# Performance work log

Hardware: AMD Instinct MI355X
Metric: run time of the kernel (lower is better)

Reference implementation:

```python
import jax, jax.numpy as jnp
import numpy as np

B, A = 8192, 16
HID, NK, NQ, NV = 256, 32, 32, 128
IN_DIM, CUR_HID, CUR_OUT, N_ACT = 512, 512, 128, 64
EXT_LAMBD, INT_LAMBD = 1.0, 0.5


def setup_inputs() -> dict:
    key = jax.random.key(0)
    ks = jax.random.split(key, 16)
    def w(k, i, o):
        return jax.random.normal(k, (i, o), jnp.float32) / np.sqrt(i)
    return {
        'x': jax.random.normal(ks[0], (B * A, IN_DIM), jnp.float32),
        'hidden': jax.random.normal(ks[1], (B, A, HID), jnp.float32),
        'Wk': w(ks[2], HID, NK), 'bk': jnp.zeros((NK,), jnp.float32),
        'Wv': w(ks[3], HID, NV), 'bv': jnp.zeros((NV,), jnp.float32),
        'Wq': w(ks[4], HID, NQ), 'bq': jnp.zeros((NQ,), jnp.float32),
        'Wa': w(ks[5], NQ + NK * A, A), 'ba': jnp.zeros((A,), jnp.float32),
        'Wt1': w(ks[6], IN_DIM, CUR_HID), 'bt1': jnp.zeros((CUR_HID,), jnp.float32),
        'Wt2': w(ks[7], CUR_HID, CUR_OUT), 'bt2': jnp.zeros((CUR_OUT,), jnp.float32),
        'Wp1': w(ks[8], IN_DIM, CUR_HID), 'bp1': jnp.zeros((CUR_HID,), jnp.float32),
        'Wp2': w(ks[9], CUR_HID, CUR_HID), 'bp2': jnp.zeros((CUR_HID,), jnp.float32),
        'Wp3': w(ks[10], CUR_HID, CUR_OUT), 'bp3': jnp.zeros((CUR_OUT,), jnp.float32),
        'Wc': w(ks[11], NV + HID, HID), 'bc': jnp.zeros((HID,), jnp.float32),
        'W2': w(ks[12], HID, N_ACT), 'b2': jnp.zeros((N_ACT,), jnp.float32),
    }


def _aggregate(x, hidden, Wk, bk, Wv, bv, Wq, bq, Wa, ba, Wt1, bt1, Wt2, bt2,
               Wp1, bp1, Wp2, bp2, Wp3, bp3, Wc, bc, W2, b2):
    # communicate(): per-agent key / value / query projections
    key_ = hidden @ Wk + bk          # [B, A, NK]
    value = hidden @ Wv + bv         # [B, A, NV]
    query = hidden @ Wq + bq         # [B, A, NQ]
    # torch.cat([key[:, i, :] for i in range(A)], -1) == reshape; repeat == broadcast
    flat_key = key_.reshape(B, A * NK)
    qk = jnp.concatenate(
        [query, jnp.broadcast_to(flat_key[:, None, :], (B, A, A * NK))], axis=-1)
    attn_weights = jax.nn.softmax(qk @ Wa + ba, axis=-1)   # [B, A, A]
    # intrinsic-motivation predictors (dropout p=0.5 in eval mode -> identity)
    tar = jax.nn.relu(x @ Wt1 + bt1) @ Wt2 + bt2           # [B*A, CUR_OUT]
    pred = jax.nn.relu(x @ Wp1 + bp1)
    pred = jax.nn.relu(pred @ Wp2 + bp2)
    pred = pred @ Wp3 + bp3
    int_imp = jnp.mean((tar - pred) ** 2, axis=-1).reshape(B, A)
    int_imp = jax.nn.softmax(int_imp, axis=-1)             # [B, A]
    # view(B,A,1).repeat(1,1,A).permute(0,2,1): out[b,i,j] = int_imp[b,j]
    int_mat = jnp.broadcast_to(int_imp[:, None, :], (B, A, A))
    attn = EXT_LAMBD * attn_weights + INT_LAMBD * jax.lax.stop_gradient(int_mat)
    applied = jnp.einsum('bij,bjv->biv', attn, value)      # [B, A, NV]
    comb = jax.nn.relu(jnp.concatenate([applied, hidden], axis=-1) @ Wc + bc)
    return comb @ W2 + b2                                  # [B, A, N_ACT]


def reference(x, hidden, Wk, bk, Wv, bv, Wq, bq, Wa, ba, Wt1, bt1, Wt2, bt2,
              Wp1, bp1, Wp2, bp2, Wp3, bp3, Wc, bc, W2, b2):
    return _aggregate(x, hidden, Wk, bk, Wv, bv, Wq, bq, Wa, ba, Wt1, bt1,
                      Wt2, bt2, Wp1, bp1, Wp2, bp2, Wp3, bp3, Wc, bc, W2, b2)
```

## Files before the change

### kernel.cpp

```cpp
#include <hip/hip_runtime.h>
#include <cstddef>
#include <cstdint>

typedef unsigned short ushort_t;
typedef __attribute__((ext_vector_type(4))) float f32x4;
typedef __attribute__((ext_vector_type(8))) short bf16x8;

#define BB   8192
#define AA   16
#define BA   131072
#define HID  256
#define NV   128

__device__ __forceinline__ float bf2f(ushort_t u) {
    union { float f; uint32_t i; } v; v.i = ((uint32_t)u) << 16; return v.f;
}
__device__ __forceinline__ ushort_t f2bf(float f) {
    union { float f; uint32_t i; } v; v.f = f;
    uint32_t r = v.i + 0x7fffu + ((v.i >> 16) & 1u);
    return (ushort_t)(r >> 16);
}
__device__ __forceinline__ void gload_lds16(const void* g, void* l) {
    __builtin_amdgcn_global_load_lds(
        (const __attribute__((address_space(1))) uint32_t*)g,
        (__attribute__((address_space(3))) uint32_t*)l, 16, 0, 0);
}

__global__ __launch_bounds__(512)
void gemm256(const ushort_t* __restrict__ A, int lda,
             const ushort_t* __restrict__ A2, int lda2, int ksplit,
             const ushort_t* __restrict__ Bt,
             const float* __restrict__ bias,
             ushort_t* __restrict__ C, int ldc, int K, int lgx, int rpx)
{
    __shared__ ushort_t lds[65536];

    const int tid  = threadIdx.x;
    const int w    = tid >> 6;
    const int lane = tid & 63;
    const int wm   = w >> 2;
    const int wn   = w & 3;
    const int fr   = lane & 15;
    const int fq   = lane >> 4;

    const int bid  = blockIdx.x;
    const int xcd  = bid & 7;
    const int slot = bid >> 3;
    const int x    = slot & ((1 << lgx) - 1);
    const int y    = xcd * rpx + (slot >> lgx);
    const size_t brow = (size_t)y * 256;
    const int    bcol = x * 256;

    const int NT = K >> 5;

    f32x4 acc[8][4];
#pragma unroll
    for (int m = 0; m < 8; ++m)
#pragma unroll
        for (int n = 0; n < 4; ++n) acc[m][n] = (f32x4){0.f, 0.f, 0.f, 0.f};

    auto stage = [&](int buf, int k0) {
        const int base = buf << 14;
#pragma unroll
        for (int r = 0; r < 4; ++r) {
            const int gamma = r * 512 + tid;
            const int gi    = gamma & 1023;
            const int row   = gi >> 2;
            const int g     = gi & 3;
            const int s     = (row ^ (row >> 2)) & 3;
            const int col   = ((g ^ s) << 3);
            const ushort_t* src;
            if (gamma >= 1024) {
                src = Bt + (size_t)(bcol + row) * K + k0 + col;
            } else if (k0 >= ksplit) {
                src = A2 + (brow + row) * (size_t)lda2 + (k0 - ksplit) + col;
            } else {
                src = A  + (brow + row) * (size_t)lda  + k0 + col;
            }
            gload_lds16(src, &lds[base + gamma * 8]);
        }
    };

    stage(0, 0);
    if (NT > 1) stage(1, 32);
    if (NT > 2) stage(2, 64);

    const int sa = (fr ^ (fr >> 2)) & 3;
    const int pc = ((fq ^ sa) & 3) << 3;

    for (int t = 0; t < NT; ++t) {
        if (t + 3 <= NT)      asm volatile("s_waitcnt vmcnt(8)" ::: "memory");
        else if (t + 2 == NT) asm volatile("s_waitcnt vmcnt(4)" ::: "memory");
        else                  asm volatile("s_waitcnt vmcnt(0)" ::: "memory");
        __builtin_amdgcn_s_barrier();
        if (t + 3 < NT) stage((t + 3) & 3, (t + 3) << 5);

        const int base = (t & 3) << 14;
        bf16x8 a[8], b[4];
#pragma unroll
        for (int m = 0; m < 8; ++m)
            a[m] = *(const bf16x8*)&lds[base + (wm * 128 + m * 16 + fr) * 32 + pc];
#pragma unroll
        for (int n = 0; n < 4; ++n)
            b[n] = *(const bf16x8*)&lds[base + 8192 + (wn * 64 + n * 16 + fr) * 32 + pc];

        __builtin_amdgcn_s_setprio(1);
#pragma unroll
        for (int m = 0; m < 8; ++m)
#pragma unroll
            for (int n = 0; n < 4; ++n)
                acc[m][n] = __builtin_amdgcn_mfma_f32_16x16x32_bf16(
                    a[m], b[n], acc[m][n], 0, 0, 0);
        __builtin_amdgcn_s_setprio(0);
    }

#pragma unroll
    for (int m = 0; m < 8; ++m) {
        const size_t rowb = brow + wm * 128 + m * 16 + fq * 4;
#pragma unroll
        for (int n = 0; n < 4; ++n) {
            const int col = bcol + wn * 64 + n * 16 + fr;
            const float bv = bias[col];
#pragma unroll
            for (int r = 0; r < 4; ++r) {
                float v = fmaxf(acc[m][n][r] + bv, 0.f);
                C[(rowb + r) * (size_t)ldc + col] = f2bf(v);
            }
        }
    }
}

template<bool OBF16, bool RELU>
__global__ __launch_bounds__(256)
void gemm_mfma(const ushort_t* __restrict__ A, int lda,
               const ushort_t* __restrict__ A2, int lda2, int ksplit,
               const ushort_t* __restrict__ Bt,
               const float* __restrict__ bias,
               void* __restrict__ C, int ldc, int N, int K, int lgx)
{
    __shared__ ushort_t As[2][128 * 64];
    __shared__ ushort_t Bs[2][128 * 64];

    const int tid  = threadIdx.x;
    const int w    = tid >> 6;
    const int lane = tid & 63;
    const int wm   = w >> 1;
    const int wn   = w & 1;

    const int bid  = blockIdx.x;
    const int xcd  = bid & 7;
    const int slot = bid >> 3;
    const int x    = slot & ((1 << lgx) - 1);
    const int y    = xcd * 128 + (slot >> lgx);
    const size_t brow = (size_t)y * 128;
    const int    bcol = x * 128;

    const int fr   = lane & 15;
    const int fq   = lane >> 4;
    const int srow = lane >> 3;
    const int scol = (lane & 7) << 3;

    f32x4 acc[4][4];
#pragma unroll
    for (int i = 0; i < 4; ++i)
#pragma unroll
        for (int j = 0; j < 4; ++j) acc[i][j] = (f32x4){0.f, 0.f, 0.f, 0.f};

    const int NT = K >> 6;

    auto stage = [&](int buf, int k0) {
#pragma unroll
        for (int i = 0; i < 4; ++i) {
            const int c = (w << 2) + i;
            const int r = (c << 3) + srow;
            const ushort_t* asrc;
            if (k0 >= ksplit)
                asrc = A2 + (brow + r) * (size_t)lda2 + (k0 - ksplit) + scol;
            else
                asrc = A  + (brow + r) * (size_t)lda  + k0 + scol;
            gload_lds16(asrc, &As[buf][(c << 9) + lane * 8]);
            gload_lds16(Bt + (size_t)(bcol + r) * K + k0 + scol,
                        &Bs[buf][(c << 9) + lane * 8]);
        }
    };

    stage(0, 0);
    __syncthreads();

    for (int t = 0; t < NT; ++t) {
        const int cur = t & 1;
        if (t + 1 < NT) stage(cur ^ 1, (t + 1) << 6);
#pragma unroll
        for (int kk = 0; kk < 2; ++kk) {
            bf16x8 a[4], b[4];
#pragma unroll
            for (int f = 0; f < 4; ++f) {
                a[f] = *(const bf16x8*)&As[cur][(wm * 64 + f * 16 + fr) * 64 + kk * 32 + fq * 8];
                b[f] = *(const bf16x8*)&Bs[cur][(wn * 64 + f * 16 + fr) * 64 + kk * 32 + fq * 8];
            }
#pragma unroll
            for (int fm = 0; fm < 4; ++fm)
#pragma unroll
                for (int fn = 0; fn < 4; ++fn)
                    acc[fm][fn] = __builtin_amdgcn_mfma_f32_16x16x32_bf16(
                        a[fm], b[fn], acc[fm][fn], 0, 0, 0);
        }
        __syncthreads();
    }

#pragma unroll
    for (int fm = 0; fm < 4; ++fm) {
        const size_t rowb = brow + wm * 64 + fm * 16 + fq * 4;
#pragma unroll
        for (int fn = 0; fn < 4; ++fn) {
            const int col = bcol + wn * 64 + fn * 16 + fr;
            if (col < N) {
                const float bv = bias[col];
#pragma unroll
                for (int r = 0; r < 4; ++r) {
                    float v = acc[fm][fn][r] + bv;
                    if (RELU) v = fmaxf(v, 0.f);
                    const size_t idx = (rowb + r) * (size_t)ldc + col;
                    if (OBF16) ((ushort_t*)C)[idx] = f2bf(v);
                    else       ((float*)C)[idx]    = v;
                }
            }
        }
    }
}

__global__ __launch_bounds__(256)
void transpose_w(const float* __restrict__ W, ushort_t* __restrict__ Wt,
                 int K, int N, int Npad)
{
    int idx = blockIdx.x * 256 + threadIdx.x;
    if (idx >= Npad * K) return;
    int n = idx / K, k = idx - n * K;
    float v = (n < N) ? W[(size_t)k * N + n] : 0.f;
    Wt[idx] = f2bf(v);
}

__global__ __launch_bounds__(256)
void transpose_wk(const float* __restrict__ W, ushort_t* __restrict__ Wt,
                  int Ksrc, int N, int ldk, int kOff, float sign)
{
    int idx = blockIdx.x * 256 + threadIdx.x;
    if (idx >= N * Ksrc) return;
    int n = idx / Ksrc, k = idx - n * Ksrc;
    Wt[(size_t)n * ldk + kOff + k] = f2bf(sign * W[(size_t)k * N + n]);
}

__global__ __launch_bounds__(256)
void conv_f32_bf16(const float* __restrict__ src, ushort_t* __restrict__ dst)
{
    size_t q = (size_t)blockIdx.x * 256 + threadIdx.x;
    float4 v = ((const float4*)src)[q];
    ushort_t* d = dst + q * 4;
    d[0] = f2bf(v.x); d[1] = f2bf(v.y); d[2] = f2bf(v.z); d[3] = f2bf(v.w);
}

__global__ void pack_bias(const float* __restrict__ bk, const float* __restrict__ bq,
                          const float* __restrict__ bv, float* __restrict__ pb)
{
    int j = threadIdx.x;
    float v = 0.f;
    if      (j < 32)  v = bk[j];
    else if (j < 64)  v = bq[j - 32];
    else if (j < 192) v = bv[j - 64];
    pb[j] = v;
}

__global__ void make_cbias(const float* __restrict__ bt2, const float* __restrict__ bp3,
                           float* __restrict__ cb)
{
    int j = threadIdx.x;
    cb[j] = bt2[j] - bp3[j];
}

__global__ __launch_bounds__(64)
void mse_softmax(const ushort_t* __restrict__ diff, float* __restrict__ int_imp)
{
    const int b = blockIdx.x, lane = threadIdx.x;
    __shared__ float m[AA];
    for (int a = 0; a < AA; ++a) {
        const uint32_t u = *(const uint32_t*)(diff + ((size_t)b * AA + a) * 128 + lane * 2);
        float d0 = bf2f((ushort_t)(u & 0xffff));
        float d1 = bf2f((ushort_t)(u >> 16));
        float s = d0 * d0 + d1 * d1;
#pragma unroll
        for (int off = 32; off > 0; off >>= 1) s += __shfl_down(s, off);
        if (lane == 0) m[a] = s * (1.f / 128.f);
    }
    __syncthreads();
    if (lane == 0) {
        float mx = -1e30f;
#pragma unroll
        for (int a = 0; a < AA; ++a) mx = fmaxf(mx, m[a]);
        float e[AA], den = 0.f;
#pragma unroll
        for (int a = 0; a < AA; ++a) { e[a] = __expf(m[a] - mx); den += e[a]; }
        float inv = 1.f / den;
#pragma unroll
        for (int a = 0; a < AA; ++a) int_imp[(size_t)b * AA + a] = e[a] * inv;
    }
}

__global__ __launch_bounds__(256)
void attn_apply(const ushort_t* __restrict__ kvq, const float* __restrict__ Wa,
                const float* __restrict__ ba, const float* __restrict__ iimp,
                ushort_t* __restrict__ applied)
{
    const int b = blockIdx.x, t = threadIdx.x;
    __shared__ float klds[512], qlds[512];
    __shared__ ushort_t vlds[2048];
    __shared__ float part[16][17];
    __shared__ float kp[16];
    __shared__ float attn[16][17];

    for (int i = t; i < 512; i += 256) {
        int a = i >> 5, c = i & 31;
        const size_t base = ((size_t)b * AA + a) * 192;
        klds[i] = bf2f(kvq[base + c]);
        qlds[i] = bf2f(kvq[base + 32 + c]);
    }
    for (int i = t; i < 2048; i += 256) {
        int j = i >> 7, v = i & 127;
        vlds[i] = kvq[((size_t)b * AA + j) * 192 + 64 + v];
    }
    __syncthreads();

    {
        int j = t & 15, seg = t >> 4;
        float s = 0.f;
        for (int c = seg * 32; c < seg * 32 + 32; ++c)
            s += klds[c] * Wa[(32 + c) * 16 + j];
        part[j][seg] = s;
    }
    __syncthreads();
    if (t < 16) {
        float s = 0.f;
#pragma unroll
        for (int seg = 0; seg < 16; ++seg) s += part[t][seg];
        kp[t] = s;
    }
    __syncthreads();

    {
        int i = t >> 4, j = t & 15;
        float s = 0.f;
#pragma unroll
        for (int q = 0; q < 32; ++q) s += qlds[i * 32 + q] * Wa[q * 16 + j];
        attn[i][j] = s + kp[j] + ba[j];
    }
    __syncthreads();
    if (t < 16) {
        float mx = -1e30f;
#pragma unroll
        for (int j = 0; j < 16; ++j) mx = fmaxf(mx, attn[t][j]);
        float e[16], den = 0.f;
#pragma unroll
        for (int j = 0; j < 16; ++j) { e[j] = __expf(attn[t][j] - mx); den += e[j]; }
        float inv = 1.f / den;
#pragma unroll
        for (int j = 0; j < 16; ++j)
            attn[t][j] = e[j] * inv + 0.5f * iimp[b * 16 + j];
    }
    __syncthreads();

    for (int o = t; o < 2048; o += 256) {
        int i = o >> 7, v = o & 127;
        float s = 0.f;
#pragma unroll
        for (int j = 0; j < 16; ++j) s += attn[i][j] * bf2f(vlds[j * 128 + v]);
        applied[((size_t)b * AA + i) * 128 + v] = f2bf(s);
    }
}

extern "C" void kernel_launch(void* const* d_in, const int* in_sizes, int n_in,
                              void* d_out, int out_size, void* d_ws, size_t ws_size,
                              hipStream_t stream)
{
    const float* x      = (const float*)d_in[0];
    const float* hidden = (const float*)d_in[1];
    const float* Wk  = (const float*)d_in[2];
    const float* bk  = (const float*)d_in[3];
    const float* Wv  = (const float*)d_in[4];
    const float* bv  = (const float*)d_in[5];
    const float* Wq  = (const float*)d_in[6];
    const float* bq  = (const float*)d_in[7];
    const float* Wa  = (const float*)d_in[8];
    const float* ba  = (const float*)d_in[9];
    const float* Wt1 = (const float*)d_in[10];
    const float* bt1 = (const float*)d_in[11];
    const float* Wt2 = (const float*)d_in[12];
    const float* bt2 = (const float*)d_in[13];
    const float* Wp1 = (const float*)d_in[14];
    const float* bp1 = (const float*)d_in[15];
    const float* Wp2 = (const float*)d_in[16];
    const float* bp2 = (const float*)d_in[17];
    const float* Wp3 = (const float*)d_in[18];
    const float* bp3 = (const float*)d_in[19];
    const float* Wc  = (const float*)d_in[20];
    const float* bc  = (const float*)d_in[21];
    const float* W2  = (const float*)d_in[22];
    const float* b2  = (const float*)d_in[23];

    float*    out = (float*)d_out;
    ushort_t* ws  = (ushort_t*)d_ws;

    ushort_t* xb  = ws;
    ushort_t* ht  = xb + (size_t)BA * 512;
    ushort_t* hp1 = ht + (size_t)BA * 1024;
    ushort_t* WT  = hp1 + (size_t)BA * 512;
    ushort_t* diff    = xb;
    ushort_t* kvq     = xb + (size_t)BA * 128;
    ushort_t* hiddenb = hp1;
    ushort_t* applied = ht;
    ushort_t* comb    = ht + (size_t)BA * 512;

    ushort_t* Wt1t = WT;
    ushort_t* Wp1t = Wt1t + 512 * 512;
    ushort_t* Wp2t = Wp1t + 512 * 512;
    ushort_t* Dt   = Wp2t + 512 * 512;
    ushort_t* Wkvq = Dt   + 128 * 1024;
    ushort_t* Wct  = Wkvq + 256 * 256;
    ushort_t* W2t  = Wct  + 256 * 384;
    float* pbias = (float*)(W2t + 128 * 256);
    float* cbias = pbias + 256;
    float* iimp  = cbias + 128;

    const dim3 blk(256);
    const int BIG = 1 << 30;

    conv_f32_bf16<<<65536, blk, 0, stream>>>(x, xb);
    transpose_w<<<1024, blk, 0, stream>>>(Wt1, Wt1t, 512, 512, 512);
    transpose_w<<<1024, blk, 0, stream>>>(Wp1, Wp1t, 512, 512, 512);
    transpose_w<<<1024, blk, 0, stream>>>(Wp2, Wp2t, 512, 512, 512);
    transpose_wk<<<256, blk, 0, stream>>>(Wt2, Dt, 512, 128, 1024, 0,    1.f);
    transpose_wk<<<256, blk, 0, stream>>>(Wp3, Dt, 512, 128, 1024, 512, -1.f);
    transpose_w<<<32,  blk, 0, stream>>>(Wk, Wkvq + 0 * 256,   256, 32, 32);
    transpose_w<<<32,  blk, 0, stream>>>(Wq, Wkvq + 32 * 256,  256, 32, 32);
    transpose_w<<<128, blk, 0, stream>>>(Wv, Wkvq + 64 * 256,  256, 128, 128);
    transpose_w<<<64,  blk, 0, stream>>>(Wk, Wkvq + 192 * 256, 256, 0, 64);
    transpose_w<<<384, blk, 0, stream>>>(Wc, Wct, 384, 256, 256);
    transpose_w<<<128, blk, 0, stream>>>(W2, W2t, 256, 64, 128);
    pack_bias<<<1, 256, 0, stream>>>(bk, bq, bv, pbias);
    make_cbias<<<1, 128, 0, stream>>>(bt2, bp3, cbias);

    gemm256<<<1024, 512, 0, stream>>>(xb, 512, xb, 512, BIG, Wt1t, bt1, ht,       1024, 512, 1, 64);
    gemm256<<<1024, 512, 0, stream>>>(xb, 512, xb, 512, BIG, Wp1t, bp1, hp1,       512, 512, 1, 64);
    gemm256<<<1024, 512, 0, stream>>>(hp1, 512, hp1, 512, BIG, Wp2t, bp2, ht + 512, 1024, 512, 1, 64);
    conv_f32_bf16<<<32768, blk, 0, stream>>>(hidden, hiddenb);
    gemm_mfma<true, false><<<1024, blk, 0, stream>>>(ht, 1024, ht, 1024, BIG, Dt, cbias, diff, 128, 128, 1024, 0);
    mse_softmax<<<BB, 64, 0, stream>>>(diff, iimp);

    gemm_mfma<true, false><<<2048, blk, 0, stream>>>(hiddenb, 256, hiddenb, 256, BIG, Wkvq, pbias, kvq, 192, 192, 256, 1);
    attn_apply<<<BB, blk, 0, stream>>>(kvq, Wa, ba, iimp, applied);

    gemm256<<<512, 512, 0, stream>>>(applied, 128, hiddenb, 256, 128, Wct, bc, comb, 256, 384, 0, 64);
    gemm_mfma<false, false><<<1024, blk, 0, stream>>>(comb, 256, comb, 256, BIG, W2t, b2, out, 64, 64, 256, 0);
}
```

Before: 694.3 us.

## Fuse x conversion into merged Wt1/Wp1 GEMM and restructure gemm256 pipeline

The standalone fp32-to-bf16 conversion of x is removed. The first-layer Wt1 and Wp1 GEMMs are merged into one N=1024 GEMM that reads fp32 x directly, converting through registers into LDS. gemm256's 4-stage async global-to-LDS pipeline becomes a 2-buffer register-staged pipeline with a __syncthreads each iteration. This saves a full x round-trip and reads x once instead of twice, but may lose latency hiding in the main GEMMs.

```diff
diff --git a/kernel.cpp b/kernel.cpp
--- a/kernel.cpp
+++ b/kernel.cpp
@@ -9,8 +9,6 @@
 #define BB   8192
 #define AA   16
 #define BA   131072
-#define HID  256
-#define NV   128
 
 __device__ __forceinline__ float bf2f(ushort_t u) {
     union { float f; uint32_t i; } v; v.i = ((uint32_t)u) << 16; return v.f;
@@ -26,14 +24,15 @@
         (__attribute__((address_space(3))) uint32_t*)l, 16, 0, 0);
 }
 
+template<bool AF32, bool RELU>
 __global__ __launch_bounds__(512)
-void gemm256(const ushort_t* __restrict__ A, int lda,
+void gemm256(const void* __restrict__ Ax, int lda,
              const ushort_t* __restrict__ A2, int lda2, int ksplit,
              const ushort_t* __restrict__ Bt,
              const float* __restrict__ bias,
              ushort_t* __restrict__ C, int ldc, int K, int lgx, int rpx)
 {
-    __shared__ ushort_t lds[65536];
+    __shared__ ushort_t lds[32768];
 
     const int tid  = threadIdx.x;
     const int w    = tid >> 6;
@@ -59,43 +58,74 @@
 #pragma unroll
         for (int n = 0; n < 4; ++n) acc[m][n] = (f32x4){0.f, 0.f, 0.f, 0.f};
 
-    auto stage = [&](int buf, int k0) {
-        const int base = buf << 14;
-#pragma unroll
-        for (int r = 0; r < 4; ++r) {
-            const int gamma = r * 512 + tid;
-            const int gi    = gamma & 1023;
-            const int row   = gi >> 2;
-            const int g     = gi & 3;
-            const int s     = (row ^ (row >> 2)) & 3;
-            const int col   = ((g ^ s) << 3);
-            const ushort_t* src;
-            if (gamma >= 1024) {
-                src = Bt + (size_t)(bcol + row) * K + k0 + col;
-            } else if (k0 >= ksplit) {
-                src = A2 + (brow + row) * (size_t)lda2 + (k0 - ksplit) + col;
-            } else {
-                src = A  + (brow + row) * (size_t)lda  + k0 + col;
+    const int arow  = tid >> 1;
+    const int ahalf = tid & 1;
+    const int as    = (arow ^ (arow >> 2)) & 3;
+    float4 areg[4];
+
+    auto stage_load = [&](int k0) {
+        const int base = ((k0 >> 5) & 1) << 14;
+#pragma unroll
+        for (int r = 0; r < 2; ++r) {
+            const int gi  = r * 512 + tid;
+            const int row = gi >> 2;
+            const int g   = gi & 3;
+            const int s   = (row ^ (row >> 2)) & 3;
+            const int col = ((g ^ s) << 3);
+            gload_lds16(Bt + (size_t)(bcol + row) * K + k0 + col,
+                        &lds[base + 8192 + gi * 8]);
+        }
+        if (AF32) {
+            const float* Af  = (const float*)Ax;
+            const float* src = Af + (brow + arow) * (size_t)lda + k0 + ahalf * 16;
+#pragma unroll
+            for (int i = 0; i < 4; ++i)
+                areg[i] = *(const float4*)(src + i * 4);
+        } else {
+#pragma unroll
+            for (int r = 0; r < 2; ++r) {
+                const int gi  = r * 512 + tid;
+                const int row = gi >> 2;
+                const int g   = gi & 3;
+                const int s   = (row ^ (row >> 2)) & 3;
+                const int col = ((g ^ s) << 3);
+                const ushort_t* src;
+                if (k0 >= ksplit)
+                    src = A2 + (brow + row) * (size_t)lda2 + (k0 - ksplit) + col;
+                else
+                    src = (const ushort_t*)Ax + (brow + row) * (size_t)lda + k0 + col;
+                gload_lds16(src, &lds[base + gi * 8]);
             }
-            gload_lds16(src, &lds[base + gamma * 8]);
         }
     };
 
-    stage(0, 0);
-    if (NT > 1) stage(1, 32);
-    if (NT > 2) stage(2, 64);
+    auto stage_write = [&](int k0) {
+        if (AF32) {
+            const int base = ((k0 >> 5) & 1) << 14;
+#pragma unroll
+            for (int j = 0; j < 2; ++j) {
+                ushort_t tmp[8];
+                const float* f = (const float*)&areg[j * 2];
+#pragma unroll
+                for (int e = 0; e < 8; ++e) tmp[e] = f2bf(f[e]);
+                const int gl = ahalf * 2 + j;
+                const int p  = gl ^ as;
+                *(bf16x8*)&lds[base + (arow * 4 + p) * 8] = *(const bf16x8*)tmp;
+            }
+        }
+    };
+
+    stage_load(0);
+    stage_write(0);
+    __syncthreads();
 
     const int sa = (fr ^ (fr >> 2)) & 3;
     const int pc = ((fq ^ sa) & 3) << 3;
 
     for (int t = 0; t < NT; ++t) {
-        if (t + 3 <= NT)      asm volatile("s_waitcnt vmcnt(8)" ::: "memory");
-        else if (t + 2 == NT) asm volatile("s_waitcnt vmcnt(4)" ::: "memory");
-        else                  asm volatile("s_waitcnt vmcnt(0)" ::: "memory");
-        __builtin_amdgcn_s_barrier();
-        if (t + 3 < NT) stage((t + 3) & 3, (t + 3) << 5);
-
-        const int base = (t & 3) << 14;
+        if (t + 1 < NT) stage_load((t + 1) << 5);
+
+        const int base = (t & 1) << 14;
         bf16x8 a[8], b[4];
 #pragma unroll
         for (int m = 0; m < 8; ++m)
@@ -112,6 +142,9 @@
                 acc[m][n] = __builtin_amdgcn_mfma_f32_16x16x32_bf16(
                     a[m], b[n], acc[m][n], 0, 0, 0);
         __builtin_amdgcn_s_setprio(0);
+
+        if (t + 1 < NT) stage_write((t + 1) << 5);
+        __syncthreads();
     }
 
 #pragma unroll
@@ -123,7 +156,8 @@
             const float bv = bias[col];
 #pragma unroll
             for (int r = 0; r < 4; ++r) {
-                float v = fmaxf(acc[m][n][r] + bv, 0.f);
+                float v = acc[m][n][r] + bv;
+                if (RELU) v = fmaxf(v, 0.f);
                 C[(rowb + r) * (size_t)ldc + col] = f2bf(v);
             }
         }
@@ -257,6 +291,14 @@
     float4 v = ((const float4*)src)[q];
     ushort_t* d = dst + q * 4;
     d[0] = f2bf(v.x); d[1] = f2bf(v.y); d[2] = f2bf(v.z); d[3] = f2bf(v.w);
+}
+
+__global__ void pack_cat2(const float* __restrict__ a, const float* __restrict__ b,
+                          float* __restrict__ o)
+{
+    int j = blockIdx.x * 256 + threadIdx.x;
+    if (j < 512) o[j] = a[j];
+    else if (j < 1024) o[j] = b[j - 512];
 }
 
 __global__ void pack_bias(const float* __restrict__ bk, const float* __restrict__ bq,
@@ -408,33 +450,31 @@
     float*    out = (float*)d_out;
     ushort_t* ws  = (ushort_t*)d_ws;
 
-    ushort_t* xb  = ws;
-    ushort_t* ht  = xb + (size_t)BA * 512;
-    ushort_t* hp1 = ht + (size_t)BA * 1024;
-    ushort_t* WT  = hp1 + (size_t)BA * 512;
-    ushort_t* diff    = xb;
-    ushort_t* kvq     = xb + (size_t)BA * 128;
-    ushort_t* hiddenb = hp1;
-    ushort_t* applied = ht;
-    ushort_t* comb    = ht + (size_t)BA * 512;
-
-    ushort_t* Wt1t = WT;
-    ushort_t* Wp1t = Wt1t + 512 * 512;
-    ushort_t* Wp2t = Wp1t + 512 * 512;
+    ushort_t* ht2  = ws;
+    ushort_t* hp2  = ht2 + (size_t)BA * 1024;
+    ushort_t* diff = hp2 + (size_t)BA * 512;
+    ushort_t* WT   = diff + (size_t)BA * 128;
+    ushort_t* kvq     = ht2;
+    ushort_t* applied = ht2 + (size_t)BA * 192;
+    ushort_t* comb    = ht2 + (size_t)BA * 320;
+    ushort_t* hiddenb = hp2;
+
+    ushort_t* Bg1  = WT;
+    ushort_t* Wp2t = Bg1  + 1024 * 512;
     ushort_t* Dt   = Wp2t + 512 * 512;
     ushort_t* Wkvq = Dt   + 128 * 1024;
     ushort_t* Wct  = Wkvq + 256 * 256;
     ushort_t* W2t  = Wct  + 256 * 384;
-    float* pbias = (float*)(W2t + 128 * 256);
-    float* cbias = pbias + 256;
-    float* iimp  = cbias + 128;
+    float* g1bias = (float*)(W2t + 128 * 256);
+    float* pbias  = g1bias + 1024;
+    float* cbias  = pbias + 256;
+    float* iimp   = cbias + 128;
 
     const dim3 blk(256);
     const int BIG = 1 << 30;
 
-    conv_f32_bf16<<<65536, blk, 0, stream>>>(x, xb);
-    transpose_w<<<1024, blk, 0, stream>>>(Wt1, Wt1t, 512, 512, 512);
-    transpose_w<<<1024, blk, 0, stream>>>(Wp1, Wp1t, 512, 512, 512);
+    transpose_w<<<1024, blk, 0, stream>>>(Wt1, Bg1,             512, 512, 512);
+    transpose_w<<<1024, blk, 0, stream>>>(Wp1, Bg1 + 512 * 512, 512, 512, 512);
     transpose_w<<<1024, blk, 0, stream>>>(Wp2, Wp2t, 512, 512, 512);
     transpose_wk<<<256, blk, 0, stream>>>(Wt2, Dt, 512, 128, 1024, 0,    1.f);
     transpose_wk<<<256, blk, 0, stream>>>(Wp3, Dt, 512, 128, 1024, 512, -1.f);
@@ -444,19 +484,25 @@
     transpose_w<<<64,  blk, 0, stream>>>(Wk, Wkvq + 192 * 256, 256, 0, 64);
     transpose_w<<<384, blk, 0, stream>>>(Wc, Wct, 384, 256, 256);
     transpose_w<<<128, blk, 0, stream>>>(W2, W2t, 256, 64, 128);
+    pack_cat2<<<4, 256, 0, stream>>>(bt1, bp1, g1bias);
     pack_bias<<<1, 256, 0, stream>>>(bk, bq, bv, pbias);
     make_cbias<<<1, 128, 0, stream>>>(bt2, bp3, cbias);
 
-    gemm256<<<1024, 512, 0, stream>>>(xb, 512, xb, 512, BIG, Wt1t, bt1, ht,       1024, 512, 1, 64);
-    gemm256<<<1024, 512, 0, stream>>>(xb, 512, xb, 512, BIG, Wp1t, bp1, hp1,       512, 512, 1, 64);
-    gemm256<<<1024, 512, 0, stream>>>(hp1, 512, hp1, 512, BIG, Wp2t, bp2, ht + 512, 1024, 512, 1, 64);
+    gemm256<true, true><<<2048, 512, 0, stream>>>(
+        x, 512, nullptr, 0, BIG, Bg1, g1bias, ht2, 1024, 512, 2, 64);
+    gemm256<false, true><<<1024, 512, 0, stream>>>(
+        ht2 + 512, 1024, nullptr, 0, BIG, Wp2t, bp2, hp2, 512, 512, 1, 64);
+    gemm_mfma<true, false><<<1024, blk, 0, stream>>>(
+        ht2, 1024, hp2, 512, 512, Dt, cbias, diff, 128, 128, 1024, 0);
+    mse_softmax<<<BB, 64, 0, stream>>>(diff, iimp);
+
     conv_f32_bf16<<<32768, blk, 0, stream>>>(hidden, hiddenb);
-    gemm_mfma<true, false><<<1024, blk, 0, stream>>>(ht, 1024, ht, 1024, BIG, Dt, cbias, diff, 128, 128, 1024, 0);
-    mse_softmax<<<BB, 64, 0, stream>>>(diff, iimp);
-
-    gemm_mfma<true, false><<<2048, blk, 0, stream>>>(hiddenb, 256, hiddenb, 256, BIG, Wkvq, pbias, kvq, 192, 192, 256, 1);
+    gemm_mfma<true, false><<<2048, blk, 0, stream>>>(
+        hiddenb, 256, hiddenb, 256, BIG, Wkvq, pbias, kvq, 192, 192, 256, 1);
     attn_apply<<<BB, blk, 0, stream>>>(kvq, Wa, ba, iimp, applied);
 
-    gemm256<<<512, 512, 0, stream>>>(applied, 128, hiddenb, 256, 128, Wct, bc, comb, 256, 384, 0, 64);
-    gemm_mfma<false, false><<<1024, blk, 0, stream>>>(comb, 256, comb, 256, BIG, W2t, b2, out, 64, 64, 256, 0);
-}
+    gemm256<false, true><<<512, 512, 0, stream>>>(
+        applied, 128, hiddenb, 256, 128, Wct, bc, comb, 256, 384, 0, 64);
+    gemm_mfma<false, false><<<1024, blk, 0, stream>>>(
+        comb, 256, comb, 256, BIG, W2t, b2, out, 64, 64, 256, 0);
+}
```

New measurement: 702.1 us. Within noise of the previous version (+1.1%).
